# Optimization experiments

Hardware: AMD Instinct MI355X
Metric: run time of the kernel (lower is better)

The kernel has to match this reference:

```python
import jax, jax.numpy as jnp
import numpy as np

_EPS = 0.001
_NINF = jnp.finfo(jnp.float32).min

B, LU, LE, D, H, HD = 4, 1024, 1024, 512, 8, 64


def setup_inputs() -> dict:
    ks = jax.random.split(jax.random.key(0), 16)
    w = 1.0 / np.sqrt(D)
    inp = {
        'u_enc': jax.random.normal(ks[0], (B, LU, D), jnp.float32),
        'e_enc': jax.random.normal(ks[1], (B, LE, D), jnp.float32),
        'logit_bpp': jax.random.normal(ks[2], (LU, LE), jnp.float32),
        'ue_mask': jax.random.bernoulli(ks[3], 0.9, (B, 1, LU, LE)),
        'eu_mask': jax.random.bernoulli(ks[4], 0.9, (B, 1, LE, LU)),
        'wq_k': jax.random.normal(ks[5], (D, H, HD), jnp.float32) * w,
        'wq_b': jnp.zeros((H, HD), jnp.float32),
        'wk_k': jax.random.normal(ks[6], (D, H, HD), jnp.float32) * w,
        'wk_b': jnp.zeros((H, HD), jnp.float32),
        'wv_k': jax.random.normal(ks[7], (D, H, HD), jnp.float32) * w,
        'wv_b': jnp.zeros((H, HD), jnp.float32),
        'wo_k': jax.random.normal(ks[8], (H, HD, D), jnp.float32) * (1.0 / np.sqrt(H * HD)),
        'wo_b': jnp.zeros((D,), jnp.float32),
        'bpp_w': jnp.float32(1.0),
        'bpp_b': jnp.float32(0.0),
    }
    return inp


def reference(u_enc, e_enc, logit_bpp, ue_mask, eu_mask,
              wq_k, wq_b, wk_k, wk_b, wv_k, wv_b, wo_k, wo_b,
              bpp_w, bpp_b):
    scale = jnp.reciprocal(jnp.sqrt(jnp.float32(HD)))
    # projections: [B, L, D] @ [D, H, HD] -> [B, L, H, HD]
    q_u = scale * (jnp.einsum('bld,dhk->blhk', u_enc, wq_k) + wq_b)
    q_e = scale * (jnp.einsum('bld,dhk->blhk', e_enc, wq_k) + wq_b)
    k_u = jnp.einsum('bld,dhk->blhk', u_enc, wk_k) + wk_b
    k_e = jnp.einsum('bld,dhk->blhk', e_enc, wk_k) + wk_b

    bpp = bpp_w * logit_bpp + bpp_b                 # [LU, LE]
    bpp_t = bpp.T                                   # [LE, LU]

    # scores: [B, H, Q, K]
    ue_w = jnp.einsum('bqhd,bkhd->bhqk', q_u, k_e) + bpp[None, None]
    eu_w = jnp.einsum('bqhd,bkhd->bhqk', q_e, k_u) + bpp_t[None, None]

    ue_w = jax.nn.softmax(ue_w + (~ue_mask) * _NINF + _EPS, axis=-1)
    eu_w = jax.nn.softmax(eu_w + (~eu_mask) * _NINF + _EPS, axis=-1)

    # deterministic path: no dropout; post-softmax re-mask
    ue_w = ue_mask * ue_w
    eu_w = eu_mask * eu_w

    v_u = jnp.einsum('bld,dhk->blhk', u_enc, wv_k) + wv_b
    v_e = jnp.einsum('bld,dhk->blhk', e_enc, wv_k) + wv_b

    u_ctx = jnp.einsum('bhqk,bkhd->bqhd', ue_w, v_e)
    e_ctx = jnp.einsum('bhqk,bkhd->bqhd', eu_w, v_u)

    u_update = jnp.einsum('bqhd,hde->bqe', u_ctx, wo_k) + wo_b
    e_update = jnp.einsum('bqhd,hde->bqe', e_ctx, wo_k) + wo_b
    return (u_update, e_update)
```

## Files before the change

### kernel.cpp

```cpp
#include <hip/hip_runtime.h>
#include <hip/hip_bf16.h>
#include <cstdint>

typedef unsigned short u16;
typedef __attribute__((ext_vector_type(8))) short short8;
typedef __attribute__((ext_vector_type(4))) float floatx4;

#define MFMA16(a, b, c) __builtin_amdgcn_mfma_f32_16x16x32_bf16(a, b, c, 0, 0, 0)
#define LOG2E 1.4426950408889634f

__device__ __forceinline__ float fast_exp2(float x) {
#if __has_builtin(__builtin_amdgcn_exp2f)
  return __builtin_amdgcn_exp2f(x);
#else
  return exp2f(x);
#endif
}
__device__ __forceinline__ u16 f2bf(float v) {
  union { float f; unsigned u; } x; x.f = v;
  unsigned r = x.u + 0x7FFF + ((x.u >> 16) & 1);
  return (u16)(r >> 16);
}
__device__ __forceinline__ float bf2f(u16 v) {
  union { unsigned u; float f; } x; x.u = ((unsigned)v) << 16; return x.f;
}
__device__ __forceinline__ void gload_lds16(const u16* g, u16* l) {
  __builtin_amdgcn_global_load_lds(
      (const __attribute__((address_space(1))) unsigned int*)(g),
      (__attribute__((address_space(3))) unsigned int*)(l), 16, 0, 0);
}

#if __has_builtin(__builtin_amdgcn_permlane32_swap) && __has_builtin(__builtin_amdgcn_permlane16_swap)
#define HAVE_PL 1
#endif
__device__ __forceinline__ void plswap32(unsigned& x, unsigned& y) {
#ifdef HAVE_PL
  auto r = __builtin_amdgcn_permlane32_swap(x, y, false, false);
  x = r[0]; y = r[1];
#else
  unsigned sx = (unsigned)__shfl_xor((int)x, 32, 64);
  unsigned sy = (unsigned)__shfl_xor((int)y, 32, 64);
  bool hi = (threadIdx.x & 32) != 0;
  unsigned nx = hi ? sy : x;
  unsigned ny = hi ? y : sx;
  x = nx; y = ny;
#endif
}
__device__ __forceinline__ void plswap16(unsigned& x, unsigned& y) {
#ifdef HAVE_PL
  auto r = __builtin_amdgcn_permlane16_swap(x, y, false, false);
  x = r[0]; y = r[1];
#else
  unsigned sx = (unsigned)__shfl_xor((int)x, 16, 64);
  unsigned sy = (unsigned)__shfl_xor((int)y, 16, 64);
  bool odd = (threadIdx.x & 16) != 0;
  unsigned nx = odd ? sy : x;
  unsigned ny = odd ? y : sx;
  x = nx; y = ny;
#endif
}

__global__ __launch_bounds__(256) void prep(
    const float* __restrict__ u, const float* __restrict__ e,
    const float* __restrict__ wq, const float* __restrict__ wk,
    const float* __restrict__ wv, const float* __restrict__ wo,
    const float* __restrict__ bq, const float* __restrict__ bk,
    const float* __restrict__ bv, const float* __restrict__ bo,
    const float* __restrict__ bpp,
    const int* __restrict__ mu, const int* __restrict__ me,
    const float* __restrict__ bw_p, const float* __restrict__ bb_p,
    u16* __restrict__ ab, u16* __restrict__ Wt,
    float* __restrict__ bias_all, u16* __restrict__ bm) {
  __shared__ float smemf[2176];
  __shared__ u16 smemo[2048];
  const int bid = blockIdx.x, t = threadIdx.x;
  if (bid < 4096) {
    int half = bid >> 11;
    int i = ((bid & 2047) * 256 + t) * 4;
    const float* s = half ? e : u;
    float4 v = *(const float4*)(s + i);
    ushort4 o = make_ushort4(f2bf(v.x), f2bf(v.y), f2bf(v.z), f2bf(v.w));
    *(ushort4*)(ab + (size_t)half * 2097152 + i) = o;
  } else if (bid < 5120) {
    int i = bid - 4096;
    int z = i >> 8, rem = i & 255;
    const float* src = z == 0 ? wq : z == 1 ? wk : z == 2 ? wv : wo;
    float scale = z == 0 ? 0.125f * LOG2E : 1.0f;
    u16* dst = Wt + (size_t)z * 262144;
    int k0 = (rem & 15) * 32, n0 = (rem >> 4) * 32;
    int tx = t & 31, ty = t >> 5;
    float (*tl)[33] = (float(*)[33])smemf;
#pragma unroll
    for (int j = 0; j < 32; j += 8) tl[ty + j][tx] = src[(size_t)(k0 + ty + j) * 512 + n0 + tx];
    __syncthreads();
#pragma unroll
    for (int j = 0; j < 32; j += 8)
      dst[(size_t)(n0 + ty + j) * 512 + k0 + tx] = f2bf(scale * tl[tx][ty + j]);
  } else if (bid < 5128) {
    int n = (bid - 5120) * 256 + t;
    float val = n < 512 ? 0.125f * LOG2E * bq[n]
              : n < 1024 ? bk[n - 512]
              : n < 1536 ? bv[n - 1024] : bo[n - 1536];
    bias_all[n] = val;
  } else {
    int i = bid - 5128;
    int kcpair = i & 7, q16 = (i >> 3) & 63, sb = i >> 9;
    int side = sb >> 2, b = sb & 3;
    const int* mask = side ? me : mu;
    const float sw = (*bw_p) * LOG2E, sb2 = (*bb_p) * LOG2E;
    if (side) {
#pragma unroll
      for (int ii = 0; ii < 2; ++ii) {
        int s = t + ii * 256;
        int rowk = s >> 2, c4 = (s & 3) * 4;
        float4 v = *(const float4*)(bpp + (size_t)(kcpair * 128 + rowk) * 1024 + q16 * 16 + c4);
        smemf[rowk * 17 + c4 + 0] = v.x;
        smemf[rowk * 17 + c4 + 1] = v.y;
        smemf[rowk * 17 + c4 + 2] = v.z;
        smemf[rowk * 17 + c4 + 3] = v.w;
      }
    }
    __syncthreads();
#pragma unroll
    for (int ii = 0; ii < 2; ++ii) {
      int s = t + ii * 256;
      int q_loc = s >> 5;
      int kq = (s & 31) * 4;
      int qg = q16 * 16 + q_loc;
      int4 mv = *(const int4*)(mask + ((size_t)b * 1024 + qg) * 1024 + kcpair * 128 + kq);
      float bvv[4];
      if (side) {
#pragma unroll
        for (int j = 0; j < 4; ++j) bvv[j] = smemf[(kq + j) * 17 + q_loc];
      } else {
        float4 v = *(const float4*)(bpp + (size_t)qg * 1024 + kcpair * 128 + kq);
        bvv[0] = v.x; bvv[1] = v.y; bvv[2] = v.z; bvv[3] = v.w;
      }
      int mm[4] = {mv.x, mv.y, mv.z, mv.w};
      int kc_loc = kq >> 6, k_loc = kq & 63;
      int kb = k_loc >> 4, within = k_loc & 15;
      int quad = within >> 2;
      int lane = q_loc + 16 * quad;
      u16 o[4];
#pragma unroll
      for (int j = 0; j < 4; ++j) o[j] = f2bf(mm[j] ? sw * bvv[j] + sb2 : -1e30f);
      *(ushort4*)&smemo[kc_loc * 1024 + lane * 16 + kb * 4] = *(const ushort4*)o;
    }
    __syncthreads();
    u16* dst = bm + (((size_t)sb * 64 + q16) * 16 + kcpair * 2) * 1024;
    *(short8*)(dst + t * 8) = *(const short8*)&smemo[t * 8];
  }
}

template <int MODE>
__global__ __launch_bounds__(256) void gemm_mfma(
    const u16* __restrict__ A, const u16* __restrict__ Bt,
    const float* __restrict__ bias, float* __restrict__ outf,
    u16* __restrict__ q_o, u16* __restrict__ k_o, u16* __restrict__ v_o) {
  __shared__ u16 As[128 * 32];
  __shared__ u16 Bs[128 * 32];
  const int t = threadIdx.x, lane = t & 63, wave = t >> 6;
  const int l15 = lane & 15, quad = lane >> 4;
  const int wy = wave >> 1, wx = wave & 1;
  const int m0 = blockIdx.x * 128, n0 = blockIdx.y * 128;
  const int K = 512;

  floatx4 zero4 = {0.f, 0.f, 0.f, 0.f};
  floatx4 acc[4][4];
#pragma unroll
  for (int mi = 0; mi < 4; ++mi)
#pragma unroll
    for (int ni = 0; ni < 4; ++ni) acc[mi][ni] = zero4;

  for (int k0 = 0; k0 < K; k0 += 32) {
    __syncthreads();
    {
      int s = t;
#pragma unroll
      for (int i = 0; i < 2; ++i, s += 256) {
        int row = s >> 2, seg = s & 3;
        gload_lds16(A + (size_t)(m0 + row) * K + k0 + seg * 8, &As[s * 8]);
      }
      s = t;
#pragma unroll
      for (int i = 0; i < 2; ++i, s += 256) {
        int row = s >> 2, seg = s & 3;
        gload_lds16(Bt + (size_t)(n0 + row) * K + k0 + seg * 8, &Bs[s * 8]);
      }
    }
    __syncthreads();
    short8 af[4], bf[4];
#pragma unroll
    for (int mi = 0; mi < 4; ++mi)
      af[mi] = *(const short8*)&As[(wy * 64 + mi * 16 + l15) * 32 + quad * 8];
#pragma unroll
    for (int ni = 0; ni < 4; ++ni)
      bf[ni] = *(const short8*)&Bs[(wx * 64 + ni * 16 + l15) * 32 + quad * 8];
#pragma unroll
    for (int mi = 0; mi < 4; ++mi)
#pragma unroll
      for (int ni = 0; ni < 4; ++ni) acc[mi][ni] = MFMA16(af[mi], bf[ni], acc[mi][ni]);
  }

#pragma unroll
  for (int mi = 0; mi < 4; ++mi)
#pragma unroll
    for (int ni = 0; ni < 4; ++ni) {
      int n = n0 + wx * 64 + ni * 16 + l15;
      float bv = bias[n];
#pragma unroll
      for (int r = 0; r < 4; ++r) {
        int m = m0 + wy * 64 + mi * 16 + quad * 4 + r;
        float v = acc[mi][ni][r] + bv;
        if (MODE == 1) {
          outf[(size_t)m * 512 + n] = v;
        } else {
          int sel = n >> 9, c = n & 511;
          u16 hv = f2bf(v);
          if (sel == 0) q_o[(size_t)m * 512 + c] = hv;
          else if (sel == 1) k_o[(size_t)m * 512 + c] = hv;
          else v_o[(size_t)m * 512 + c] = hv;
        }
      }
    }
}

__global__ __launch_bounds__(256) void vt_trans(const u16* __restrict__ v_all,
                                                u16* __restrict__ vt_all) {
  __shared__ u16 tl[64][72];
  int z = blockIdx.z, half = z >> 2, b = z & 3, h = blockIdx.y, l0 = blockIdx.x * 64;
  const u16* src = v_all + (size_t)half * 2097152;
  u16* dst = vt_all + (size_t)half * 2097152;
  int t = threadIdx.x;
#pragma unroll
  for (int i = 0; i < 2; ++i) {
    int s = t + i * 256, row = s >> 3, seg = s & 7;
    *(short8*)&tl[row][seg * 8] =
        *(const short8*)(src + (size_t)(b * 1024 + l0 + row) * 512 + h * 64 + seg * 8);
  }
  __syncthreads();
#pragma unroll
  for (int i = 0; i < 2; ++i) {
    int s = t + i * 256, hd = s >> 3, seg = s & 7;
    u16 tmp[8];
#pragma unroll
    for (int j = 0; j < 8; ++j) tmp[j] = tl[seg * 8 + j][hd];
    *(short8*)(dst + ((size_t)(b * 8 + h) * 64 + hd) * 1024 + l0 + seg * 8) =
        *(const short8*)tmp;
  }
}

__global__ __launch_bounds__(256) void attn_mfma(
    const u16* __restrict__ q_all, const u16* __restrict__ k_all,
    const u16* __restrict__ vt_all, const u16* __restrict__ bm_all,
    u16* __restrict__ ctx_all) {
  __shared__ u16 Ks[2][64 * 64];
  __shared__ u16 Vs[2][64 * 64];
  __shared__ u16 epi[4][32 * 72];
  const int t = threadIdx.x, lane = t & 63, wave = t >> 6;
  const int l15 = lane & 15, quad = lane >> 4;

  const int f = blockIdx.x;
  const int g = f & 7, r0 = f >> 3;
  const int combo = g * 8 + (r0 >> 3);
  const int x = r0 & 7;
  const int side = combo >> 5, b = (combo >> 3) & 3, h = combo & 7;

  const size_t HALF = 2097152;
  const u16* Q = q_all + side * HALF;
  const u16* K = k_all + (1 - side) * HALF;
  const u16* Vt = vt_all + (1 - side) * HALF;
  const u16* bm = bm_all + side * (size_t)4194304;
  u16* ctx = ctx_all + side * HALF;
  const int qbase = x * 128 + wave * 32;
  const int q16g = qbase >> 4;

  short8 qb[2][2];
#pragma unroll
  for (int s = 0; s < 2; ++s) {
    const u16* qp = Q + (size_t)(b * 1024 + qbase + s * 16 + l15) * 512 + h * 64 + quad * 8;
    qb[s][0] = *(const short8*)qp;
    qb[s][1] = *(const short8*)(qp + 32);
  }

  short8 onesA;
#pragma unroll
  for (int j = 0; j < 8; ++j) onesA[j] = (short)0x3F80;

  floatx4 Oc[4][2];
  floatx4 Dacc[2];
#pragma unroll
  for (int s = 0; s < 2; ++s) {
    Dacc[s] = (floatx4){0.f, 0.f, 0.f, 0.f};
#pragma unroll
    for (int nb = 0; nb < 4; ++nb) Oc[nb][s] = (floatx4){0.f, 0.f, 0.f, 0.f};
  }

#define STAGE(buf, k0)                                                             \
  {                                                                                \
    _Pragma("unroll") for (int i = 0; i < 2; ++i) {                                \
      int s = t + i * 256, row = s >> 3, pseg = s & 7, lseg = pseg ^ (row & 7);    \
      gload_lds16(K + (size_t)(b * 1024 + (k0) + row) * 512 + h * 64 + lseg * 8,   \
                  &Ks[buf][s * 8]);                                                \
      gload_lds16(Vt + ((size_t)(b * 8 + h) * 64 + row) * 1024 + (k0) + lseg * 8,  \
                  &Vs[buf][s * 8]);                                                \
    }                                                                              \
  }

  STAGE(0, 0)

  for (int it = 0; it < 16; ++it) {
    const int cur = it & 1;
    __syncthreads();
    if (it < 15) STAGE(cur ^ 1, it * 64 + 64)

    short8 bmv[2][2];
#pragma unroll
    for (int s = 0; s < 2; ++s) {
      const u16* bp = bm + ((((size_t)b * 64 + q16g + s) * 16 + it) * 64 + lane) * 16;
      bmv[s][0] = *(const short8*)bp;
      bmv[s][1] = *(const short8*)(bp + 8);
    }

    floatx4 St[2][4];
#pragma unroll
    for (int s = 0; s < 2; ++s)
#pragma unroll
      for (int kb = 0; kb < 4; ++kb) St[s][kb] = (floatx4){-64.f, -64.f, -64.f, -64.f};
#pragma unroll
    for (int kb = 0; kb < 4; ++kb) {
      int krow = kb * 16 + l15;
      short8 kf0 = *(const short8*)&Ks[cur][krow * 64 + ((quad ^ (krow & 7)) * 8)];
      short8 kf1 = *(const short8*)&Ks[cur][krow * 64 + (((4 + quad) ^ (krow & 7)) * 8)];
#pragma unroll
      for (int s = 0; s < 2; ++s) {
        St[s][kb] = MFMA16(kf0, qb[s][0], St[s][kb]);
        St[s][kb] = MFMA16(kf1, qb[s][1], St[s][kb]);
      }
    }

    unsigned pka[2][4], pkb[2][4];
#pragma unroll
    for (int s = 0; s < 2; ++s)
#pragma unroll
      for (int kb = 0; kb < 4; ++kb) {
        float pv[4];
#pragma unroll
        for (int r = 0; r < 4; ++r) {
          int i = kb * 4 + r;
          float bmf = bf2f((u16)((i < 8) ? bmv[s][0][i] : bmv[s][1][i - 8]));
          pv[r] = fast_exp2(St[s][kb][r] + bmf);
        }
        union { __hip_bfloat162 h; unsigned u; } c0, c1;
        c0.h = __float22bfloat162_rn(make_float2(pv[0], pv[1]));
        c1.h = __float22bfloat162_rn(make_float2(pv[2], pv[3]));
        pka[s][kb] = c0.u;
        pkb[s][kb] = c1.u;
      }

    short8 Pb[2][2];
#pragma unroll
    for (int s = 0; s < 2; ++s)
#pragma unroll
      for (int ks = 0; ks < 2; ++ks) {
        unsigned a0 = pka[s][2 * ks], a1 = pka[s][2 * ks + 1];
        unsigned b0 = pkb[s][2 * ks], b1 = pkb[s][2 * ks + 1];
        plswap32(a0, a1); plswap16(a0, a1);
        plswap32(b0, b1); plswap16(b0, b1);
        union { short8 s8; unsigned u[4]; } fb;
        fb.u[0] = a0; fb.u[1] = b0; fb.u[2] = a1; fb.u[3] = b1;
        Pb[s][ks] = fb.s8;
        Dacc[s] = MFMA16(onesA, fb.s8, Dacc[s]);
      }

#pragma unroll
    for (int nb = 0; nb < 4; ++nb) {
      int vrow = nb * 16 + l15;
#pragma unroll
      for (int ks = 0; ks < 2; ++ks) {
        short8 vf = *(const short8*)&Vs[cur][vrow * 64 + ((((ks * 4 + quad)) ^ (vrow & 7)) * 8)];
        Oc[nb][0] = MFMA16(vf, Pb[0][ks], Oc[nb][0]);
        Oc[nb][1] = MFMA16(vf, Pb[1][ks], Oc[nb][1]);
      }
    }
  }

  u16* eb = &epi[wave][0];
#pragma unroll
  for (int s = 0; s < 2; ++s) {
    float dv = Dacc[s][0];
    float inv = dv > 0.f ? 1.f / dv : 0.f;
#pragma unroll
    for (int nb = 0; nb < 4; ++nb) {
      union { __hip_bfloat162 h; unsigned u; } w0, w1;
      w0.h = __float22bfloat162_rn(make_float2(Oc[nb][s][0] * inv, Oc[nb][s][1] * inv));
      w1.h = __float22bfloat162_rn(make_float2(Oc[nb][s][2] * inv, Oc[nb][s][3] * inv));
      union { unsigned u[2]; unsigned long long ull; } pk;
      pk.u[0] = w0.u; pk.u[1] = w1.u;
      *(unsigned long long*)&eb[(s * 16 + l15) * 72 + nb * 16 + quad * 4] = pk.ull;
    }
  }
#pragma unroll
  for (int p = 0; p < 4; ++p) {
    int row = p * 8 + (lane >> 3);
    int cs = (lane & 7) * 8;
    short8 v = *(const short8*)&eb[row * 72 + cs];
    *(short8*)(ctx + (size_t)(b * 1024 + qbase + row) * 512 + h * 64 + cs) = v;
  }
}

extern "C" void kernel_launch(void* const* d_in, const int* in_sizes, int n_in,
                              void* d_out, int out_size, void* d_ws, size_t ws_size,
                              hipStream_t stream) {
  const float* u_enc = (const float*)d_in[0];
  const float* e_enc = (const float*)d_in[1];
  const float* logit_bpp = (const float*)d_in[2];
  const int* ue_mask = (const int*)d_in[3];
  const int* eu_mask = (const int*)d_in[4];
  const float* wq_k = (const float*)d_in[5];
  const float* wq_b = (const float*)d_in[6];
  const float* wk_k = (const float*)d_in[7];
  const float* wk_b = (const float*)d_in[8];
  const float* wv_k = (const float*)d_in[9];
  const float* wv_b = (const float*)d_in[10];
  const float* wo_k = (const float*)d_in[11];
  const float* wo_b = (const float*)d_in[12];
  const float* bpp_w = (const float*)d_in[13];
  const float* bpp_b = (const float*)d_in[14];

  float* out = (float*)d_out;

  u16* ws16 = (u16*)d_ws;
  u16* ab    = ws16;
  u16* Wt    = ab + 4194304;
  u16* q_all = Wt + 1048576;
  u16* k_all = q_all + 4194304;
  u16* v_all = k_all + 4194304;
  u16* ctx   = v_all + 4194304;
  u16* bm    = ctx + 4194304;
  float* bias_all = (float*)(bm + 8388608);
  u16* vt = ab;

  prep<<<9224, 256, 0, stream>>>(u_enc, e_enc, wq_k, wk_k, wv_k, wo_k,
                                 wq_b, wk_b, wv_b, wo_b, logit_bpp,
                                 ue_mask, eu_mask, bpp_w, bpp_b,
                                 ab, Wt, bias_all, bm);
  gemm_mfma<0><<<dim3(64, 12), 256, 0, stream>>>(ab, Wt, bias_all, nullptr,
                                                 q_all, k_all, v_all);
  vt_trans<<<dim3(16, 8, 8), 256, 0, stream>>>(v_all, vt);
  attn_mfma<<<512, 256, 0, stream>>>(q_all, k_all, vt, bm, ctx);
  gemm_mfma<1><<<dim3(64, 4), 256, 0, stream>>>(ctx, Wt + 786432, bias_all + 1536,
                                                out, nullptr, nullptr, nullptr);
}
```

Before: 197.3 us.

## Fuse V transpose into projection GEMM epilogue and widen K tile with swizzled LDS

Removes the separate vt_trans kernel by having the QKV projection GEMM write V directly in transposed per-head layout. The transpose is staged through the now-free LDS tiles. The GEMM main loop also moves from a K step of 32 to 64, halving barrier count, and XOR-swizzles LDS columns to avoid bank conflicts. The cost is double the LDS per block, which may reduce occupancy, plus extra epilogue complexity for the V tiles.

Result: no change. 200.5 us (+1.6%).

```diff
diff --git a/kernel.cpp b/kernel.cpp
--- a/kernel.cpp
+++ b/kernel.cpp
@@ -156,97 +156,107 @@
 __global__ __launch_bounds__(256) void gemm_mfma(
     const u16* __restrict__ A, const u16* __restrict__ Bt,
     const float* __restrict__ bias, float* __restrict__ outf,
-    u16* __restrict__ q_o, u16* __restrict__ k_o, u16* __restrict__ v_o) {
-  __shared__ u16 As[128 * 32];
-  __shared__ u16 Bs[128 * 32];
+    u16* __restrict__ q_o, u16* __restrict__ k_o, u16* __restrict__ vt_o) {
+  __shared__ u16 As[128 * 64];
+  __shared__ u16 Bs[128 * 64];
   const int t = threadIdx.x, lane = t & 63, wave = t >> 6;
   const int l15 = lane & 15, quad = lane >> 4;
   const int wy = wave >> 1, wx = wave & 1;
   const int m0 = blockIdx.x * 128, n0 = blockIdx.y * 128;
   const int K = 512;
 
-  floatx4 zero4 = {0.f, 0.f, 0.f, 0.f};
   floatx4 acc[4][4];
 #pragma unroll
   for (int mi = 0; mi < 4; ++mi)
 #pragma unroll
-    for (int ni = 0; ni < 4; ++ni) acc[mi][ni] = zero4;
-
-  for (int k0 = 0; k0 < K; k0 += 32) {
-    __syncthreads();
-    {
-      int s = t;
-#pragma unroll
-      for (int i = 0; i < 2; ++i, s += 256) {
-        int row = s >> 2, seg = s & 3;
-        gload_lds16(A + (size_t)(m0 + row) * K + k0 + seg * 8, &As[s * 8]);
-      }
-      s = t;
-#pragma unroll
-      for (int i = 0; i < 2; ++i, s += 256) {
-        int row = s >> 2, seg = s & 3;
-        gload_lds16(Bt + (size_t)(n0 + row) * K + k0 + seg * 8, &Bs[s * 8]);
-      }
-    }
-    __syncthreads();
-    short8 af[4], bf[4];
+    for (int ni = 0; ni < 4; ++ni) acc[mi][ni] = (floatx4){0.f, 0.f, 0.f, 0.f};
+
+  for (int k0 = 0; k0 < K; k0 += 64) {
+    __syncthreads();
+#pragma unroll
+    for (int i = 0; i < 4; ++i) {
+      int s = t + i * 256, row = s >> 3, seg = s & 7;
+      gload_lds16(A + (size_t)(m0 + row) * K + k0 + ((seg ^ (row & 7)) * 8),
+                  &As[s * 8]);
+    }
+#pragma unroll
+    for (int i = 0; i < 4; ++i) {
+      int s = t + i * 256, row = s >> 3, seg = s & 7;
+      gload_lds16(Bt + (size_t)(n0 + row) * K + k0 + ((seg ^ (row & 7)) * 8),
+                  &Bs[s * 8]);
+    }
+    __syncthreads();
+#pragma unroll
+    for (int kh = 0; kh < 2; ++kh) {
+      short8 af[4], bf[4];
+#pragma unroll
+      for (int mi = 0; mi < 4; ++mi) {
+        int row = wy * 64 + mi * 16 + l15;
+        af[mi] = *(const short8*)&As[row * 64 + (((kh * 4 + quad) ^ (row & 7)) * 8)];
+      }
+#pragma unroll
+      for (int ni = 0; ni < 4; ++ni) {
+        int row = wx * 64 + ni * 16 + l15;
+        bf[ni] = *(const short8*)&Bs[row * 64 + (((kh * 4 + quad) ^ (row & 7)) * 8)];
+      }
+#pragma unroll
+      for (int mi = 0; mi < 4; ++mi)
+#pragma unroll
+        for (int ni = 0; ni < 4; ++ni) acc[mi][ni] = MFMA16(af[mi], bf[ni], acc[mi][ni]);
+    }
+  }
+
+  if (MODE == 0 && n0 >= 1024) {
+    __syncthreads();
+    u16* eb = (wave < 2) ? (As + wave * 4096) : (Bs + (wave - 2) * 4096);
+    const int b = m0 >> 10, l0 = m0 & 1023;
+    const int h = ((n0 - 1024) >> 6) + wx;
+#pragma unroll
+    for (int pass = 0; pass < 2; ++pass) {
+#pragma unroll
+      for (int nj = 0; nj < 2; ++nj) {
+        int ni = pass * 2 + nj;
+        int np = nj * 16 + l15;
+        int n = n0 + wx * 64 + ni * 16 + l15;
+        float bv = bias[n];
+        u16 o[4];
+#pragma unroll
+        for (int mi = 0; mi < 4; ++mi) {
+#pragma unroll
+          for (int r = 0; r < 4; ++r) o[r] = f2bf(acc[mi][ni][r] + bv);
+          *(uint2*)&eb[np * 72 + mi * 16 + quad * 4] = *(const uint2*)o;
+        }
+      }
+#pragma unroll
+      for (int sp = 0; sp < 4; ++sp) {
+        int row = sp * 8 + (lane >> 3);
+        int col = (lane & 7) * 8;
+        short8 v = *(const short8*)&eb[row * 72 + col];
+        *(short8*)(vt_o + ((size_t)(b * 8 + h) * 64 + pass * 32 + row) * 1024 +
+                   l0 + wy * 64 + col) = v;
+      }
+    }
+  } else {
 #pragma unroll
     for (int mi = 0; mi < 4; ++mi)
-      af[mi] = *(const short8*)&As[(wy * 64 + mi * 16 + l15) * 32 + quad * 8];
-#pragma unroll
-    for (int ni = 0; ni < 4; ++ni)
-      bf[ni] = *(const short8*)&Bs[(wx * 64 + ni * 16 + l15) * 32 + quad * 8];
-#pragma unroll
-    for (int mi = 0; mi < 4; ++mi)
-#pragma unroll
-      for (int ni = 0; ni < 4; ++ni) acc[mi][ni] = MFMA16(af[mi], bf[ni], acc[mi][ni]);
-  }
-
-#pragma unroll
-  for (int mi = 0; mi < 4; ++mi)
-#pragma unroll
-    for (int ni = 0; ni < 4; ++ni) {
-      int n = n0 + wx * 64 + ni * 16 + l15;
-      float bv = bias[n];
-#pragma unroll
-      for (int r = 0; r < 4; ++r) {
-        int m = m0 + wy * 64 + mi * 16 + quad * 4 + r;
-        float v = acc[mi][ni][r] + bv;
-        if (MODE == 1) {
-          outf[(size_t)m * 512 + n] = v;
-        } else {
-          int sel = n >> 9, c = n & 511;
-          u16 hv = f2bf(v);
-          if (sel == 0) q_o[(size_t)m * 512 + c] = hv;
-          else if (sel == 1) k_o[(size_t)m * 512 + c] = hv;
-          else v_o[(size_t)m * 512 + c] = hv;
+#pragma unroll
+      for (int ni = 0; ni < 4; ++ni) {
+        int n = n0 + wx * 64 + ni * 16 + l15;
+        float bv = bias[n];
+#pragma unroll
+        for (int r = 0; r < 4; ++r) {
+          int m = m0 + wy * 64 + mi * 16 + quad * 4 + r;
+          float v = acc[mi][ni][r] + bv;
+          if (MODE == 1) {
+            outf[(size_t)m * 512 + n] = v;
+          } else {
+            int sel = n >> 9, c = n & 511;
+            u16 hv = f2bf(v);
+            if (sel == 0) q_o[(size_t)m * 512 + c] = hv;
+            else k_o[(size_t)m * 512 + c] = hv;
+          }
         }
       }
-    }
-}
-
-__global__ __launch_bounds__(256) void vt_trans(const u16* __restrict__ v_all,
-                                                u16* __restrict__ vt_all) {
-  __shared__ u16 tl[64][72];
-  int z = blockIdx.z, half = z >> 2, b = z & 3, h = blockIdx.y, l0 = blockIdx.x * 64;
-  const u16* src = v_all + (size_t)half * 2097152;
-  u16* dst = vt_all + (size_t)half * 2097152;
-  int t = threadIdx.x;
-#pragma unroll
-  for (int i = 0; i < 2; ++i) {
-    int s = t + i * 256, row = s >> 3, seg = s & 7;
-    *(short8*)&tl[row][seg * 8] =
-        *(const short8*)(src + (size_t)(b * 1024 + l0 + row) * 512 + h * 64 + seg * 8);
-  }
-  __syncthreads();
-#pragma unroll
-  for (int i = 0; i < 2; ++i) {
-    int s = t + i * 256, hd = s >> 3, seg = s & 7;
-    u16 tmp[8];
-#pragma unroll
-    for (int j = 0; j < 8; ++j) tmp[j] = tl[seg * 8 + j][hd];
-    *(short8*)(dst + ((size_t)(b * 8 + h) * 64 + hd) * 1024 + l0 + seg * 8) =
-        *(const short8*)tmp;
   }
 }
 
@@ -435,19 +445,17 @@
   u16* Wt    = ab + 4194304;
   u16* q_all = Wt + 1048576;
   u16* k_all = q_all + 4194304;
-  u16* v_all = k_all + 4194304;
-  u16* ctx   = v_all + 4194304;
+  u16* vt    = k_all + 4194304;
+  u16* ctx   = vt + 4194304;
   u16* bm    = ctx + 4194304;
   float* bias_all = (float*)(bm + 8388608);
-  u16* vt = ab;
 
   prep<<<9224, 256, 0, stream>>>(u_enc, e_enc, wq_k, wk_k, wv_k, wo_k,
                                  wq_b, wk_b, wv_b, wo_b, logit_bpp,
                                  ue_mask, eu_mask, bpp_w, bpp_b,
                                  ab, Wt, bias_all, bm);
   gemm_mfma<0><<<dim3(64, 12), 256, 0, stream>>>(ab, Wt, bias_all, nullptr,
-                                                 q_all, k_all, v_all);
-  vt_trans<<<dim3(16, 8, 8), 256, 0, stream>>>(v_all, vt);
+                                                 q_all, k_all, vt);
   attn_mfma<<<512, 256, 0, stream>>>(q_all, k_all, vt, bm, ctx);
   gemm_mfma<1><<<dim3(64, 4), 256, 0, stream>>>(ctx, Wt + 786432, bias_all + 1536,
                                                 out, nullptr, nullptr, nullptr);
```
